# Performance work log

Measured on AMD Instinct MI355X. Metric: run time of the kernel, lower is better.

The kernel has to match this reference:

```python
import jax, jax.numpy as jnp
import numpy as np

DIM = 256
NUM_HEADS = 8
WH, WW = 7, 7
N = WH * WW
B_ = 4096
TABLE = (2 * WH - 1) * (2 * WW - 1)  # 169


def _relative_position_index():
    ch, cw = np.meshgrid(np.arange(WH), np.arange(WW), indexing='ij')
    coords = np.stack([ch, cw]).reshape(2, -1)            # [2, N]
    rel = coords[:, :, None] - coords[:, None, :]          # [2, N, N]
    rel = rel.transpose(1, 2, 0)                           # [N, N, 2]
    rel[:, :, 0] += WH - 1
    rel[:, :, 1] += WW - 1
    rel[:, :, 0] *= 2 * WW - 1
    return jnp.asarray(rel.sum(-1), dtype=jnp.int32)       # [N, N]


def setup_inputs() -> dict:
    key = jax.random.key(0)
    ks = jax.random.split(key, 6)
    x = jax.random.normal(ks[0], (B_, N, DIM), dtype=jnp.float32)
    qkv_w = jax.random.normal(ks[1], (3 * DIM, DIM), dtype=jnp.float32) * 0.02
    qkv_b = jnp.zeros((3 * DIM,), dtype=jnp.float32)
    proj_w = jax.random.normal(ks[2], (DIM, DIM), dtype=jnp.float32) * 0.02
    proj_b = jnp.zeros((DIM,), dtype=jnp.float32)
    bias_table = jax.random.normal(ks[3], (TABLE, NUM_HEADS), dtype=jnp.float32) * 0.02
    rel_idx = _relative_position_index()
    return {"x": x, "qkv_w": qkv_w, "qkv_b": qkv_b, "proj_w": proj_w,
            "proj_b": proj_b, "bias_table": bias_table, "rel_idx": rel_idx}


def reference(x, qkv_w, qkv_b, proj_w, proj_b, bias_table, rel_idx):
    B, n, C = x.shape
    hd = C // NUM_HEADS
    scale = hd ** -0.5
    qkv = (jnp.einsum('bnc,oc->bno', x, qkv_w) + qkv_b)
    qkv = qkv.reshape(B, n, 3, NUM_HEADS, hd).transpose(2, 0, 3, 1, 4)
    q, k, v = qkv[0], qkv[1], qkv[2]
    attn = jnp.einsum('bhnd,bhmd->bhnm', q * scale, k)     # [B, H, N, N]
    # relative position bias gather: [N*N, H] -> [H, N, N]
    bias = bias_table[rel_idx.reshape(-1)].reshape(n, n, NUM_HEADS)
    attn = attn + bias.transpose(2, 0, 1)[None]
    attn = jax.nn.softmax(attn, axis=-1)
    out = jnp.einsum('bhnm,bhmd->bnhd', attn, v).reshape(B, n, C)
    out = jnp.einsum('bnc,oc->bno', out, proj_w) + proj_b
    return out
```

## Files before the change

kernel.cpp:

```cpp
#include <hip/hip_runtime.h>
#include <stdint.h>

#define NTOK 49
#define DIM 256
#define NH 8
#define HD 32
#define NWIN 4096

typedef short bf16x8 __attribute__((ext_vector_type(8)));
typedef float f32x4 __attribute__((ext_vector_type(4)));

__device__ __forceinline__ unsigned short f2bf(float f) {
    union { float f; unsigned int u; } v; v.f = f;
    unsigned int r = v.u + 0x7FFFu + ((v.u >> 16) & 1u);
    return (unsigned short)(r >> 16);
}

__device__ __forceinline__ f32x4 mfma16(bf16x8 a, bf16x8 b, f32x4 c) {
    return __builtin_amdgcn_mfma_f32_16x16x32_bf16(a, b, c, 0, 0, 0);
}

__device__ __forceinline__ bf16x8 ld8s(const unsigned short* p) {
    return *(const bf16x8*)p;
}

__global__ void prep_kernel(const float* __restrict__ qkv_w,
                            const float* __restrict__ proj_w,
                            const float* __restrict__ bias_table,
                            const int* __restrict__ rel_idx,
                            unsigned short* __restrict__ wqkv,
                            unsigned short* __restrict__ wproj,
                            float* __restrict__ biasx)
{
    int i0 = blockIdx.x * blockDim.x + threadIdx.x;
    int stride = gridDim.x * blockDim.x;
    for (int t = i0; t < 768 * 256; t += stride) wqkv[t] = f2bf(qkv_w[t]);
    for (int t = i0; t < 256 * 256; t += stride) wproj[t] = f2bf(proj_w[t]);
    for (int t = i0; t < NH * 64 * 64; t += stride) {
        int h = t >> 12;
        int m = (t >> 6) & 63;
        int n = t & 63;
        float v;
        if (n >= NTOK)      v = -1e30f;
        else if (m >= NTOK) v = 0.0f;
        else                v = bias_table[rel_idx[m * NTOK + n] * NH + h];
        biasx[t] = v;
    }
}

__global__ __launch_bounds__(256, 2) void attn_kernel(
    const float* __restrict__ x,
    const float* __restrict__ qkv_b,
    const unsigned short* __restrict__ wqkv,
    const float* __restrict__ biasx,
    unsigned short* __restrict__ aout)
{
    __shared__ unsigned short xs[64 * 264];
    __shared__ unsigned short qs[2 * 64 * 40];
    __shared__ unsigned short ks[2 * 64 * 40];
    __shared__ unsigned short vt[2 * 32 * 72];

    const int tid  = threadIdx.x;
    const int wave = tid >> 6;
    const int lane = tid & 63;
    const int l16  = lane & 15;
    const int lq   = lane >> 4;
    const int w    = blockIdx.x;
    const float scale = 0.17677669529663687f;

    const float* xw = x + (size_t)w * (NTOK * DIM);
    for (int idx = tid * 4; idx < NTOK * DIM; idx += 256 * 4) {
        float4 f = *(const float4*)(xw + idx);
        int r = idx >> 8, c = idx & 255;
        unsigned short* d = &xs[r * 264 + c];
        d[0] = f2bf(f.x); d[1] = f2bf(f.y); d[2] = f2bf(f.z); d[3] = f2bf(f.w);
    }
    for (int idx = tid; idx < 15 * 264; idx += 256)
        xs[49 * 264 + idx] = 0;
    __syncthreads();

    bf16x8 afrag[4][8];
#pragma unroll
    for (int mt = 0; mt < 4; ++mt)
#pragma unroll
        for (int c = 0; c < 8; ++c)
            afrag[mt][c] = ld8s(&xs[(mt * 16 + l16) * 264 + c * 32 + lq * 8]);

    unsigned short* Pbuf = xs;

    for (int p = 0; p < 4; ++p) {
#pragma unroll
        for (int ti = 0; ti < 3; ++ti) {
            int tl   = wave * 3 + ti;
            int grp  = tl >> 2;
            int sub  = tl & 3;
            int tile = grp * 16 + p * 4 + sub;
            int ch   = tile * 16 + l16;

            const unsigned short* bptr = wqkv + (size_t)ch * 256 + lq * 8;
            bf16x8 bfr[8];
#pragma unroll
            for (int c = 0; c < 8; ++c)
                bfr[c] = ld8s(bptr + c * 32);

            f32x4 acc[4];
#pragma unroll
            for (int mt = 0; mt < 4; ++mt) {
                f32x4 z = {0.f, 0.f, 0.f, 0.f};
                acc[mt] = z;
            }
#pragma unroll
            for (int c = 0; c < 8; ++c)
#pragma unroll
                for (int mt = 0; mt < 4; ++mt)
                    acc[mt] = mfma16(afrag[mt][c], bfr[c], acc[mt]);

            float bv  = qkv_b[ch];
            int   chm = ch & 255;
            int   hl  = (chm >> 5) & 1;
            int   d   = chm & 31;
#pragma unroll
            for (int mt = 0; mt < 4; ++mt)
#pragma unroll
                for (int r = 0; r < 4; ++r) {
                    int row = mt * 16 + lq * 4 + r;
                    float v = acc[mt][r] + bv;
                    if (grp == 0)      qs[(hl * 64 + row) * 40 + d] = f2bf(v * scale);
                    else if (grp == 1) ks[(hl * 64 + row) * 40 + d] = f2bf(v);
                    else               vt[(hl * 32 + d) * 72 + row] = f2bf(v);
                }
        }
        __syncthreads();

        {
            int hl = wave >> 1;
            int h  = 2 * p + hl;
            int mh = wave & 1;

            bf16x8 qf[2];
#pragma unroll
            for (int i = 0; i < 2; ++i)
                qf[i] = ld8s(&qs[(hl * 64 + (2 * mh + i) * 16 + l16) * 40 + lq * 8]);

            f32x4 sacc[2][4];
#pragma unroll
            for (int i = 0; i < 2; ++i)
#pragma unroll
                for (int nt = 0; nt < 4; ++nt) {
                    f32x4 z = {0.f, 0.f, 0.f, 0.f};
                    sacc[i][nt] = z;
                }
#pragma unroll
            for (int nt = 0; nt < 4; ++nt) {
                bf16x8 kf = ld8s(&ks[(hl * 64 + nt * 16 + l16) * 40 + lq * 8]);
#pragma unroll
                for (int i = 0; i < 2; ++i)
                    sacc[i][nt] = mfma16(qf[i], kf, sacc[i][nt]);
            }

            const float* bh = biasx + h * 4096;
            float pr[2][4];
#pragma unroll
            for (int i = 0; i < 2; ++i) {
                int mt = 2 * mh + i;
#pragma unroll
                for (int r = 0; r < 4; ++r) {
                    int row = mt * 16 + lq * 4 + r;
                    float s0 = sacc[i][0][r] + bh[row * 64 +  0 + l16];
                    float s1 = sacc[i][1][r] + bh[row * 64 + 16 + l16];
                    float s2 = sacc[i][2][r] + bh[row * 64 + 32 + l16];
                    float s3 = sacc[i][3][r] + bh[row * 64 + 48 + l16];
                    float mx = fmaxf(fmaxf(s0, s1), fmaxf(s2, s3));
#pragma unroll
                    for (int off = 1; off < 16; off <<= 1)
                        mx = fmaxf(mx, __shfl_xor(mx, off));
                    float e0 = __expf(s0 - mx);
                    float e1 = __expf(s1 - mx);
                    float e2 = __expf(s2 - mx);
                    float e3 = __expf(s3 - mx);
                    float sum = e0 + e1 + e2 + e3;
#pragma unroll
                    for (int off = 1; off < 16; off <<= 1)
                        sum += __shfl_xor(sum, off);
                    pr[i][r] = 1.0f / sum;
                    unsigned short* Pr = Pbuf + (hl * 64 + row) * 72;
                    Pr[ 0 + l16] = f2bf(e0);
                    Pr[16 + l16] = f2bf(e1);
                    Pr[32 + l16] = f2bf(e2);
                    Pr[48 + l16] = f2bf(e3);
                }
            }

            f32x4 oacc[2][2];
#pragma unroll
            for (int i = 0; i < 2; ++i)
#pragma unroll
                for (int nt = 0; nt < 2; ++nt) {
                    f32x4 z = {0.f, 0.f, 0.f, 0.f};
                    oacc[i][nt] = z;
                }
#pragma unroll
            for (int kc = 0; kc < 2; ++kc) {
                bf16x8 pf[2];
#pragma unroll
                for (int i = 0; i < 2; ++i)
                    pf[i] = ld8s(&Pbuf[(hl * 64 + (2 * mh + i) * 16 + l16) * 72 + kc * 32 + lq * 8]);
#pragma unroll
                for (int nt = 0; nt < 2; ++nt) {
                    bf16x8 vf = ld8s(&vt[(hl * 32 + nt * 16 + l16) * 72 + kc * 32 + lq * 8]);
#pragma unroll
                    for (int i = 0; i < 2; ++i)
                        oacc[i][nt] = mfma16(pf[i], vf, oacc[i][nt]);
                }
            }

#pragma unroll
            for (int i = 0; i < 2; ++i)
#pragma unroll
                for (int r = 0; r < 4; ++r) {
                    int row = (2 * mh + i) * 16 + lq * 4 + r;
                    if (row < NTOK) {
                        size_t base = ((size_t)w * NTOK + row) * 256 + h * 32;
                        float rs = pr[i][r];
                        aout[base +      l16] = f2bf(oacc[i][0][r] * rs);
                        aout[base + 16 + l16] = f2bf(oacc[i][1][r] * rs);
                    }
                }
        }
        __syncthreads();
    }
}

__global__ __launch_bounds__(256, 2) void proj_kernel(
    const unsigned short* __restrict__ aout,
    const unsigned short* __restrict__ wproj,
    const float* __restrict__ proj_b,
    float* __restrict__ out)
{
    __shared__ unsigned short as_[64 * 264];

    const int tid  = threadIdx.x;
    const int wave = tid >> 6;
    const int lane = tid & 63;
    const int l16  = lane & 15;
    const int lq   = lane >> 4;
    const size_t mb = blockIdx.x;

    const unsigned short* arow = aout + mb * (64 * 256);
    for (int idx = tid * 8; idx < 64 * 256; idx += 256 * 8) {
        uint4 v = *(const uint4*)(arow + idx);
        int r = idx >> 8, c = idx & 255;
        *(uint4*)&as_[r * 264 + c] = v;
    }
    __syncthreads();

    bf16x8 af[4][8];
#pragma unroll
    for (int mt = 0; mt < 4; ++mt)
#pragma unroll
        for (int c = 0; c < 8; ++c)
            af[mt][c] = ld8s(&as_[(mt * 16 + l16) * 264 + c * 32 + lq * 8]);

#pragma unroll
    for (int nt4 = 0; nt4 < 4; ++nt4) {
        int nt = wave * 4 + nt4;
        int ch = nt * 16 + l16;
        const unsigned short* bptr = wproj + (size_t)ch * 256 + lq * 8;
        bf16x8 bfr[8];
#pragma unroll
        for (int c = 0; c < 8; ++c)
            bfr[c] = ld8s(bptr + c * 32);

        f32x4 acc[4];
#pragma unroll
        for (int mt = 0; mt < 4; ++mt) {
            f32x4 z = {0.f, 0.f, 0.f, 0.f};
            acc[mt] = z;
        }
#pragma unroll
        for (int c = 0; c < 8; ++c)
#pragma unroll
            for (int mt = 0; mt < 4; ++mt)
                acc[mt] = mfma16(af[mt][c], bfr[c], acc[mt]);

        float pb = proj_b[ch];
#pragma unroll
        for (int mt = 0; mt < 4; ++mt)
#pragma unroll
            for (int r = 0; r < 4; ++r) {
                size_t row = mb * 64 + mt * 16 + lq * 4 + r;
                out[row * 256 + ch] = acc[mt][r] + pb;
            }
    }
}

extern "C" void kernel_launch(void* const* d_in, const int* in_sizes, int n_in,
                              void* d_out, int out_size, void* d_ws, size_t ws_size,
                              hipStream_t stream) {
    const float* x          = (const float*)d_in[0];
    const float* qkv_w      = (const float*)d_in[1];
    const float* qkv_b      = (const float*)d_in[2];
    const float* proj_w     = (const float*)d_in[3];
    const float* proj_b     = (const float*)d_in[4];
    const float* bias_table = (const float*)d_in[5];
    const int*   rel_idx    = (const int*)d_in[6];
    float* out = (float*)d_out;

    char* ws = (char*)d_ws;
    unsigned short* wqkv  = (unsigned short*)ws;
    unsigned short* wproj = (unsigned short*)(ws + 393216);
    float*          biasx = (float*)(ws + 524288);
    unsigned short* aout  = (unsigned short*)(ws + 655360);

    prep_kernel<<<256, 256, 0, stream>>>(qkv_w, proj_w, bias_table, rel_idx,
                                         wqkv, wproj, biasx);
    attn_kernel<<<NWIN, 256, 0, stream>>>(x, qkv_b, wqkv, biasx, aout);
    proj_kernel<<<3136, 256, 0, stream>>>(aout, wproj, proj_b, out);
}
```

Measured before the change: 768.6 us.

## Fuse output projection into attention kernel and restructure QKV/softmax paths

Merges the projection kernel into the attention kernel so each window keeps its attention output in shared memory and writes the final fp32 result directly. This removes the bf16 intermediate round trip through global memory and one launch. It also loads x straight from global into register fragments, swaps MFMA operand order for transposed packed stores, drops the softmax max subtraction, and uses packed bf16 conversions. Dropping the max relies on scores being small, which risks overflow for other inputs, and the larger shared memory footprint may reduce occupancy.

After: 695.1 us. 1.11x faster.

```diff
diff --git a/kernel.cpp b/kernel.cpp
--- a/kernel.cpp
+++ b/kernel.cpp
@@ -1,27 +1,42 @@
 #include <hip/hip_runtime.h>
+#include <hip/hip_bf16.h>
 #include <stdint.h>
 
 #define NTOK 49
-#define DIM 256
 #define NH 8
-#define HD 32
 #define NWIN 4096
 
 typedef short bf16x8 __attribute__((ext_vector_type(8)));
 typedef float f32x4 __attribute__((ext_vector_type(4)));
 
+__device__ __forceinline__ f32x4 mfma16(bf16x8 a, bf16x8 b, f32x4 c) {
+    return __builtin_amdgcn_mfma_f32_16x16x32_bf16(a, b, c, 0, 0, 0);
+}
+__device__ __forceinline__ bf16x8 ld8s(const unsigned short* p) {
+    return *(const bf16x8*)p;
+}
+__device__ __forceinline__ unsigned int pk2bf(float a, float b) {
+    __hip_bfloat162 h = __float22bfloat162_rn(float2{a, b});
+    return *reinterpret_cast<unsigned int*>(&h);
+}
+__device__ __forceinline__ void st4bf(unsigned short* p, float a, float b, float c, float d) {
+    uint2 u;
+    u.x = pk2bf(a, b);
+    u.y = pk2bf(c, d);
+    *reinterpret_cast<uint2*>(p) = u;
+}
+__device__ __forceinline__ bf16x8 pk8(float4 f0, float4 f1) {
+    union { bf16x8 v; unsigned int u[4]; } t;
+    t.u[0] = pk2bf(f0.x, f0.y);
+    t.u[1] = pk2bf(f0.z, f0.w);
+    t.u[2] = pk2bf(f1.x, f1.y);
+    t.u[3] = pk2bf(f1.z, f1.w);
+    return t.v;
+}
 __device__ __forceinline__ unsigned short f2bf(float f) {
     union { float f; unsigned int u; } v; v.f = f;
     unsigned int r = v.u + 0x7FFFu + ((v.u >> 16) & 1u);
     return (unsigned short)(r >> 16);
-}
-
-__device__ __forceinline__ f32x4 mfma16(bf16x8 a, bf16x8 b, f32x4 c) {
-    return __builtin_amdgcn_mfma_f32_16x16x32_bf16(a, b, c, 0, 0, 0);
-}
-
-__device__ __forceinline__ bf16x8 ld8s(const unsigned short* p) {
-    return *(const bf16x8*)p;
 }
 
 __global__ void prep_kernel(const float* __restrict__ qkv_w,
@@ -48,17 +63,21 @@
     }
 }
 
-__global__ __launch_bounds__(256, 2) void attn_kernel(
+__global__ __launch_bounds__(256, 2) void fused_kernel(
     const float* __restrict__ x,
     const float* __restrict__ qkv_b,
     const unsigned short* __restrict__ wqkv,
     const float* __restrict__ biasx,
-    unsigned short* __restrict__ aout)
+    const unsigned short* __restrict__ wproj,
+    const float* __restrict__ proj_b,
+    float* __restrict__ out)
 {
-    __shared__ unsigned short xs[64 * 264];
-    __shared__ unsigned short qs[2 * 64 * 40];
-    __shared__ unsigned short ks[2 * 64 * 40];
-    __shared__ unsigned short vt[2 * 32 * 72];
+    __shared__ unsigned short smem[31744];
+    unsigned short* ao = smem;
+    unsigned short* qs = smem + 16896;
+    unsigned short* ks = qs + 5120;
+    unsigned short* vt = qs + 10240;
+    unsigned short* Pb = qs;
 
     const int tid  = threadIdx.x;
     const int wave = tid >> 6;
@@ -68,26 +87,30 @@
     const int w    = blockIdx.x;
     const float scale = 0.17677669529663687f;
 
-    const float* xw = x + (size_t)w * (NTOK * DIM);
-    for (int idx = tid * 4; idx < NTOK * DIM; idx += 256 * 4) {
-        float4 f = *(const float4*)(xw + idx);
-        int r = idx >> 8, c = idx & 255;
-        unsigned short* d = &xs[r * 264 + c];
-        d[0] = f2bf(f.x); d[1] = f2bf(f.y); d[2] = f2bf(f.z); d[3] = f2bf(f.w);
+    const float* xw = x + (size_t)w * (NTOK * 256);
+    bf16x8 afrag[4][8];
+#pragma unroll
+    for (int mt = 0; mt < 4; ++mt) {
+        int tok = mt * 16 + l16;
+#pragma unroll
+        for (int c = 0; c < 8; ++c) {
+            if (tok < NTOK) {
+                const float* p = xw + tok * 256 + c * 32 + lq * 8;
+                float4 f0 = *(const float4*)p;
+                float4 f1 = *(const float4*)(p + 4);
+                afrag[mt][c] = pk8(f0, f1);
+            } else {
+                union { bf16x8 v; unsigned int u[4]; } z;
+                z.u[0] = z.u[1] = z.u[2] = z.u[3] = 0;
+                afrag[mt][c] = z.v;
+            }
+        }
     }
-    for (int idx = tid; idx < 15 * 264; idx += 256)
-        xs[49 * 264 + idx] = 0;
-    __syncthreads();
-
-    bf16x8 afrag[4][8];
-#pragma unroll
-    for (int mt = 0; mt < 4; ++mt)
-#pragma unroll
-        for (int c = 0; c < 8; ++c)
-            afrag[mt][c] = ld8s(&xs[(mt * 16 + l16) * 264 + c * 32 + lq * 8]);
-
-    unsigned short* Pbuf = xs;
-
+
+    const int hl = wave >> 1;
+    const int mh = wave & 1;
+
+#pragma unroll 1
     for (int p = 0; p < 4; ++p) {
 #pragma unroll
         for (int ti = 0; ti < 3; ++ti) {
@@ -95,202 +118,182 @@
             int grp  = tl >> 2;
             int sub  = tl & 3;
             int tile = grp * 16 + p * 4 + sub;
-            int ch   = tile * 16 + l16;
-
-            const unsigned short* bptr = wqkv + (size_t)ch * 256 + lq * 8;
+            const unsigned short* bptr = wqkv + (size_t)(tile * 16 + l16) * 256 + lq * 8;
             bf16x8 bfr[8];
 #pragma unroll
-            for (int c = 0; c < 8; ++c)
-                bfr[c] = ld8s(bptr + c * 32);
+            for (int c = 0; c < 8; ++c) bfr[c] = ld8s(bptr + c * 32);
 
             f32x4 acc[4];
 #pragma unroll
+            for (int i = 0; i < 4; ++i) { f32x4 z = {0.f,0.f,0.f,0.f}; acc[i] = z; }
+
+            if (grp < 2) {
+#pragma unroll
+                for (int c = 0; c < 8; ++c)
+#pragma unroll
+                    for (int nt = 0; nt < 4; ++nt)
+                        acc[nt] = mfma16(bfr[c], afrag[nt][c], acc[nt]);
+                int chb = tile * 16 + lq * 4;
+                float4 bv = *(const float4*)(qkv_b + chb);
+                int c0 = chb & 255;
+                int hh = (c0 >> 5) & 1, d0 = c0 & 31;
+                unsigned short* dst = (grp == 0 ? qs : ks) + (hh * 64) * 40 + d0;
+                float sc = (grp == 0) ? scale : 1.0f;
+#pragma unroll
+                for (int nt = 0; nt < 4; ++nt) {
+                    int tok = nt * 16 + l16;
+                    st4bf(dst + tok * 40,
+                          (acc[nt][0] + bv.x) * sc, (acc[nt][1] + bv.y) * sc,
+                          (acc[nt][2] + bv.z) * sc, (acc[nt][3] + bv.w) * sc);
+                }
+            } else {
+#pragma unroll
+                for (int c = 0; c < 8; ++c)
+#pragma unroll
+                    for (int mt = 0; mt < 4; ++mt)
+                        acc[mt] = mfma16(afrag[mt][c], bfr[c], acc[mt]);
+                int ch = tile * 16 + l16;
+                float bv = qkv_b[ch];
+                int c0 = ch & 255;
+                int hh = (c0 >> 5) & 1, d = c0 & 31;
+                unsigned short* dst = vt + (hh * 32 + d) * 72;
+#pragma unroll
+                for (int mt = 0; mt < 4; ++mt) {
+                    int tok0 = mt * 16 + lq * 4;
+                    st4bf(dst + tok0, acc[mt][0] + bv, acc[mt][1] + bv,
+                                      acc[mt][2] + bv, acc[mt][3] + bv);
+                }
+            }
+        }
+        __syncthreads();
+
+        const int h = 2 * p + hl;
+        bf16x8 kf[4], qf[2];
+#pragma unroll
+        for (int mt = 0; mt < 4; ++mt)
+            kf[mt] = ld8s(&ks[(hl * 64 + mt * 16 + l16) * 40 + lq * 8]);
+#pragma unroll
+        for (int ni = 0; ni < 2; ++ni)
+            qf[ni] = ld8s(&qs[(hl * 64 + mh * 32 + ni * 16 + l16) * 40 + lq * 8]);
+
+        f32x4 se[4][2];
+#pragma unroll
+        for (int mt = 0; mt < 4; ++mt)
+#pragma unroll
+            for (int ni = 0; ni < 2; ++ni) { f32x4 z = {0.f,0.f,0.f,0.f}; se[mt][ni] = z; }
+#pragma unroll
+        for (int mt = 0; mt < 4; ++mt)
+#pragma unroll
+            for (int ni = 0; ni < 2; ++ni)
+                se[mt][ni] = mfma16(kf[mt], qf[ni], se[mt][ni]);
+
+        const float* bh = biasx + (h << 12);
+        float rinv[2];
+#pragma unroll
+        for (int ni = 0; ni < 2; ++ni) {
+            int q = mh * 32 + ni * 16 + l16;
+            float lsum = 0.0f;
+#pragma unroll
             for (int mt = 0; mt < 4; ++mt) {
-                f32x4 z = {0.f, 0.f, 0.f, 0.f};
-                acc[mt] = z;
-            }
-#pragma unroll
-            for (int c = 0; c < 8; ++c)
-#pragma unroll
-                for (int mt = 0; mt < 4; ++mt)
-                    acc[mt] = mfma16(afrag[mt][c], bfr[c], acc[mt]);
-
-            float bv  = qkv_b[ch];
-            int   chm = ch & 255;
-            int   hl  = (chm >> 5) & 1;
-            int   d   = chm & 31;
+                float4 bb = *(const float4*)(bh + q * 64 + mt * 16 + lq * 4);
+                float e0 = __expf(se[mt][ni][0] + bb.x);
+                float e1 = __expf(se[mt][ni][1] + bb.y);
+                float e2 = __expf(se[mt][ni][2] + bb.z);
+                float e3 = __expf(se[mt][ni][3] + bb.w);
+                se[mt][ni][0] = e0; se[mt][ni][1] = e1;
+                se[mt][ni][2] = e2; se[mt][ni][3] = e3;
+                lsum += (e0 + e1) + (e2 + e3);
+            }
+            lsum += __shfl_xor(lsum, 16);
+            lsum += __shfl_xor(lsum, 32);
+            rinv[ni] = 1.0f / lsum;
+        }
+        __syncthreads();
+
+#pragma unroll
+        for (int ni = 0; ni < 2; ++ni) {
+            int q = mh * 32 + ni * 16 + l16;
+            float rv = rinv[ni];
 #pragma unroll
             for (int mt = 0; mt < 4; ++mt)
-#pragma unroll
-                for (int r = 0; r < 4; ++r) {
-                    int row = mt * 16 + lq * 4 + r;
-                    float v = acc[mt][r] + bv;
-                    if (grp == 0)      qs[(hl * 64 + row) * 40 + d] = f2bf(v * scale);
-                    else if (grp == 1) ks[(hl * 64 + row) * 40 + d] = f2bf(v);
-                    else               vt[(hl * 32 + d) * 72 + row] = f2bf(v);
-                }
-        }
-        __syncthreads();
-
-        {
-            int hl = wave >> 1;
-            int h  = 2 * p + hl;
-            int mh = wave & 1;
-
-            bf16x8 qf[2];
-#pragma unroll
-            for (int i = 0; i < 2; ++i)
-                qf[i] = ld8s(&qs[(hl * 64 + (2 * mh + i) * 16 + l16) * 40 + lq * 8]);
-
-            f32x4 sacc[2][4];
-#pragma unroll
-            for (int i = 0; i < 2; ++i)
-#pragma unroll
-                for (int nt = 0; nt < 4; ++nt) {
-                    f32x4 z = {0.f, 0.f, 0.f, 0.f};
-                    sacc[i][nt] = z;
-                }
-#pragma unroll
-            for (int nt = 0; nt < 4; ++nt) {
-                bf16x8 kf = ld8s(&ks[(hl * 64 + nt * 16 + l16) * 40 + lq * 8]);
-#pragma unroll
-                for (int i = 0; i < 2; ++i)
-                    sacc[i][nt] = mfma16(qf[i], kf, sacc[i][nt]);
-            }
-
-            const float* bh = biasx + h * 4096;
-            float pr[2][4];
-#pragma unroll
-            for (int i = 0; i < 2; ++i) {
-                int mt = 2 * mh + i;
-#pragma unroll
-                for (int r = 0; r < 4; ++r) {
-                    int row = mt * 16 + lq * 4 + r;
-                    float s0 = sacc[i][0][r] + bh[row * 64 +  0 + l16];
-                    float s1 = sacc[i][1][r] + bh[row * 64 + 16 + l16];
-                    float s2 = sacc[i][2][r] + bh[row * 64 + 32 + l16];
-                    float s3 = sacc[i][3][r] + bh[row * 64 + 48 + l16];
-                    float mx = fmaxf(fmaxf(s0, s1), fmaxf(s2, s3));
-#pragma unroll
-                    for (int off = 1; off < 16; off <<= 1)
-                        mx = fmaxf(mx, __shfl_xor(mx, off));
-                    float e0 = __expf(s0 - mx);
-                    float e1 = __expf(s1 - mx);
-                    float e2 = __expf(s2 - mx);
-                    float e3 = __expf(s3 - mx);
-                    float sum = e0 + e1 + e2 + e3;
-#pragma unroll
-                    for (int off = 1; off < 16; off <<= 1)
-                        sum += __shfl_xor(sum, off);
-                    pr[i][r] = 1.0f / sum;
-                    unsigned short* Pr = Pbuf + (hl * 64 + row) * 72;
-                    Pr[ 0 + l16] = f2bf(e0);
-                    Pr[16 + l16] = f2bf(e1);
-                    Pr[32 + l16] = f2bf(e2);
-                    Pr[48 + l16] = f2bf(e3);
-                }
-            }
-
-            f32x4 oacc[2][2];
-#pragma unroll
-            for (int i = 0; i < 2; ++i)
-#pragma unroll
-                for (int nt = 0; nt < 2; ++nt) {
-                    f32x4 z = {0.f, 0.f, 0.f, 0.f};
-                    oacc[i][nt] = z;
-                }
-#pragma unroll
-            for (int kc = 0; kc < 2; ++kc) {
-                bf16x8 pf[2];
-#pragma unroll
-                for (int i = 0; i < 2; ++i)
-                    pf[i] = ld8s(&Pbuf[(hl * 64 + (2 * mh + i) * 16 + l16) * 72 + kc * 32 + lq * 8]);
-#pragma unroll
-                for (int nt = 0; nt < 2; ++nt) {
-                    bf16x8 vf = ld8s(&vt[(hl * 32 + nt * 16 + l16) * 72 + kc * 32 + lq * 8]);
-#pragma unroll
-                    for (int i = 0; i < 2; ++i)
-                        oacc[i][nt] = mfma16(pf[i], vf, oacc[i][nt]);
-                }
-            }
-
-#pragma unroll
-            for (int i = 0; i < 2; ++i)
-#pragma unroll
-                for (int r = 0; r < 4; ++r) {
-                    int row = (2 * mh + i) * 16 + lq * 4 + r;
-                    if (row < NTOK) {
-                        size_t base = ((size_t)w * NTOK + row) * 256 + h * 32;
-                        float rs = pr[i][r];
-                        aout[base +      l16] = f2bf(oacc[i][0][r] * rs);
-                        aout[base + 16 + l16] = f2bf(oacc[i][1][r] * rs);
-                    }
-                }
-        }
+                st4bf(&Pb[(hl * 64 + q) * 72 + mt * 16 + lq * 4],
+                      se[mt][ni][0] * rv, se[mt][ni][1] * rv,
+                      se[mt][ni][2] * rv, se[mt][ni][3] * rv);
+        }
+        __threadfence_block();
+
+        bf16x8 vf[2][2], pf[2][2];
+#pragma unroll
+        for (int kc = 0; kc < 2; ++kc) {
+#pragma unroll
+            for (int mt = 0; mt < 2; ++mt)
+                vf[mt][kc] = ld8s(&vt[(hl * 32 + mt * 16 + l16) * 72 + kc * 32 + lq * 8]);
+#pragma unroll
+            for (int ni = 0; ni < 2; ++ni)
+                pf[ni][kc] = ld8s(&Pb[(hl * 64 + mh * 32 + ni * 16 + l16) * 72 + kc * 32 + lq * 8]);
+        }
+        f32x4 ot[2][2];
+#pragma unroll
+        for (int mt = 0; mt < 2; ++mt)
+#pragma unroll
+            for (int ni = 0; ni < 2; ++ni) { f32x4 z = {0.f,0.f,0.f,0.f}; ot[mt][ni] = z; }
+#pragma unroll
+        for (int kc = 0; kc < 2; ++kc)
+#pragma unroll
+            for (int mt = 0; mt < 2; ++mt)
+#pragma unroll
+                for (int ni = 0; ni < 2; ++ni)
+                    ot[mt][ni] = mfma16(vf[mt][kc], pf[ni][kc], ot[mt][ni]);
+
+#pragma unroll
+        for (int mt = 0; mt < 2; ++mt)
+#pragma unroll
+            for (int ni = 0; ni < 2; ++ni) {
+                int q = mh * 32 + ni * 16 + l16;
+                st4bf(&ao[q * 264 + h * 32 + mt * 16 + lq * 4],
+                      ot[mt][ni][0], ot[mt][ni][1], ot[mt][ni][2], ot[mt][ni][3]);
+            }
         __syncthreads();
     }
-}
-
-__global__ __launch_bounds__(256, 2) void proj_kernel(
-    const unsigned short* __restrict__ aout,
-    const unsigned short* __restrict__ wproj,
-    const float* __restrict__ proj_b,
-    float* __restrict__ out)
-{
-    __shared__ unsigned short as_[64 * 264];
-
-    const int tid  = threadIdx.x;
-    const int wave = tid >> 6;
-    const int lane = tid & 63;
-    const int l16  = lane & 15;
-    const int lq   = lane >> 4;
-    const size_t mb = blockIdx.x;
-
-    const unsigned short* arow = aout + mb * (64 * 256);
-    for (int idx = tid * 8; idx < 64 * 256; idx += 256 * 8) {
-        uint4 v = *(const uint4*)(arow + idx);
-        int r = idx >> 8, c = idx & 255;
-        *(uint4*)&as_[r * 264 + c] = v;
-    }
-    __syncthreads();
-
-    bf16x8 af[4][8];
-#pragma unroll
-    for (int mt = 0; mt < 4; ++mt)
+
+    bf16x8 af2[4][8];
+#pragma unroll
+    for (int nt = 0; nt < 4; ++nt)
 #pragma unroll
         for (int c = 0; c < 8; ++c)
-            af[mt][c] = ld8s(&as_[(mt * 16 + l16) * 264 + c * 32 + lq * 8]);
-
-#pragma unroll
-    for (int nt4 = 0; nt4 < 4; ++nt4) {
-        int nt = wave * 4 + nt4;
-        int ch = nt * 16 + l16;
-        const unsigned short* bptr = wproj + (size_t)ch * 256 + lq * 8;
-        bf16x8 bfr[8];
+            af2[nt][c] = ld8s(&ao[(nt * 16 + l16) * 264 + c * 32 + lq * 8]);
+
+#pragma unroll
+    for (int t4 = 0; t4 < 4; ++t4) {
+        int tile = wave * 4 + t4;
+        const unsigned short* wp = wproj + (size_t)(tile * 16 + l16) * 256 + lq * 8;
+        bf16x8 wfr[8];
+#pragma unroll
+        for (int c = 0; c < 8; ++c) wfr[c] = ld8s(wp + c * 32);
+
+        f32x4 acc[4];
+#pragma unroll
+        for (int i = 0; i < 4; ++i) { f32x4 z = {0.f,0.f,0.f,0.f}; acc[i] = z; }
 #pragma unroll
         for (int c = 0; c < 8; ++c)
-            bfr[c] = ld8s(bptr + c * 32);
-
-        f32x4 acc[4];
-#pragma unroll
-        for (int mt = 0; mt < 4; ++mt) {
-            f32x4 z = {0.f, 0.f, 0.f, 0.f};
-            acc[mt] = z;
-        }
-#pragma unroll
-        for (int c = 0; c < 8; ++c)
-#pragma unroll
-            for (int mt = 0; mt < 4; ++mt)
-                acc[mt] = mfma16(af[mt][c], bfr[c], acc[mt]);
-
-        float pb = proj_b[ch];
-#pragma unroll
-        for (int mt = 0; mt < 4; ++mt)
-#pragma unroll
-            for (int r = 0; r < 4; ++r) {
-                size_t row = mb * 64 + mt * 16 + lq * 4 + r;
-                out[row * 256 + ch] = acc[mt][r] + pb;
-            }
+#pragma unroll
+            for (int nt = 0; nt < 4; ++nt)
+                acc[nt] = mfma16(wfr[c], af2[nt][c], acc[nt]);
+
+        int chb = tile * 16 + lq * 4;
+        float4 pb = *(const float4*)(proj_b + chb);
+#pragma unroll
+        for (int nt = 0; nt < 4; ++nt) {
+            int tok = nt * 16 + l16;
+            if (tok < NTOK) {
+                float4 o;
+                o.x = acc[nt][0] + pb.x;
+                o.y = acc[nt][1] + pb.y;
+                o.z = acc[nt][2] + pb.z;
+                o.w = acc[nt][3] + pb.w;
+                *(float4*)(out + ((size_t)w * NTOK + tok) * 256 + chb) = o;
+            }
+        }
     }
 }
 
@@ -310,10 +313,9 @@
     unsigned short* wqkv  = (unsigned short*)ws;
     unsigned short* wproj = (unsigned short*)(ws + 393216);
     float*          biasx = (float*)(ws + 524288);
-    unsigned short* aout  = (unsigned short*)(ws + 655360);
 
     prep_kernel<<<256, 256, 0, stream>>>(qkv_w, proj_w, bias_table, rel_idx,
                                          wqkv, wproj, biasx);
-    attn_kernel<<<NWIN, 256, 0, stream>>>(x, qkv_b, wqkv, biasx, aout);
-    proj_kernel<<<3136, 256, 0, stream>>>(aout, wproj, proj_b, out);
-}
+    fused_kernel<<<NWIN, 256, 0, stream>>>(x, qkv_b, wqkv, biasx, wproj,
+                                           proj_b, out);
+}
```
